# Kernel tuning notes

Measured on AMD Instinct MI355X. Metric: run time of the kernel, lower is better.

The kernel has to match this reference:

```python
import jax, jax.numpy as jnp
import numpy as np

EPS = 1e-8  # torch CosineSimilarity default eps


def setup_inputs() -> dict:
    key = jax.random.key(0)
    ks = jax.random.split(key, 7)
    B, C, W, E, D = 64, 256, 256, 2048, 2048
    return {
        "x_img_dense": jax.random.normal(ks[0], (B, C, E), dtype=jnp.float32),
        "x_txt_dense": jax.random.normal(ks[1], (B, W, E), dtype=jnp.float32),
        "y_what_card_leader_choose": jax.random.normal(ks[2], (B, C), dtype=jnp.float32),
        "W_img1": jax.random.normal(ks[3], (D, E), dtype=jnp.float32) * 0.02,
        "b_img1": jax.random.normal(ks[4], (D,), dtype=jnp.float32) * 0.02,
        "W_words1": jax.random.normal(ks[5], (D, E), dtype=jnp.float32) * 0.02,
        "b_words1": jax.random.normal(ks[6], (D,), dtype=jnp.float32) * 0.02,
    }


def reference(x_img_dense, x_txt_dense, y_what_card_leader_choose,
              W_img1, b_img1, W_words1, b_words1):
    # Default path: img_layer=True, words_layer=True, comb_layer=False,
    # same_img_words_layer=False, gumbel=False, inference=False.
    xi = jnp.einsum('bce,de->bcd', x_img_dense, W_img1) + b_img1   # [B, C, D]
    xt = jnp.einsum('bwe,de->bwd', x_txt_dense, W_words1) + b_words1  # [B, W, D]

    # gather leader card embedding per batch element
    idx = jnp.argmax(y_what_card_leader_choose, axis=1)            # [B]
    leader = jnp.take_along_axis(xi, idx[:, None, None], axis=1)[:, 0, :]  # [B, D]

    # cosine similarity (dim=2 in torch): leader broadcast over words axis
    dot = jnp.einsum('bd,bwd->bw', leader, xt)                     # [B, W]
    denom = jnp.linalg.norm(leader, axis=-1, keepdims=True) * jnp.linalg.norm(xt, axis=-1)
    logits = dot / jnp.maximum(denom, EPS)                         # [B, W]

    # module returns softmax of `logits` (logits_final is dead code)
    return jax.nn.softmax(logits, axis=1)
```

## Files before the change

kernel.cpp:

```cpp
#include <hip/hip_runtime.h>
#include <hip/hip_bf16.h>
#include <stdint.h>

typedef unsigned short u16;
typedef __bf16 bf16x8 __attribute__((ext_vector_type(8)));
typedef float  f32x4  __attribute__((ext_vector_type(4)));
typedef float  fvec4  __attribute__((ext_vector_type(4)));

constexpr int NB = 64;
constexpr int NC = 256;
constexpr int NW = 256;
constexpr int NE = 2048;
constexpr int ND = 2048;
constexpr int MROWS = NB * NW;

constexpr int BM = 128, BN = 128, BK = 64;
constexpr int KSPLIT = 4;
constexpr int KSLICE = NE / KSPLIT;

constexpr int BM2 = 256, BN2 = 256;
constexpr int NT_K = NE / BK;
constexpr int NSLOT2 = ND / BN2;
constexpr int NSLOT1 = ND / BN;

constexpr size_t OFF_IDX  = 0;
constexpr size_t OFF_PART = 256;
constexpr size_t OFF_DOTP = 2097408;
constexpr size_t OFF_SSQP = 3145984;
constexpr size_t OFF_WW   = 4194560;
constexpr size_t OFF_XT   = 12583168;
constexpr size_t NEED_FULL = OFF_XT + 67108864ull;

__device__ __forceinline__ u16 f2bf(float f) {
    uint32_t u = __float_as_uint(f);
    u += 0x7fffu + ((u >> 16) & 1u);
    return (u16)(u >> 16);
}

__global__ void k_conv_argmax(const float* __restrict__ a, u16* __restrict__ da, int n4a,
                              const float* __restrict__ b, u16* __restrict__ db, int n4b,
                              const float* __restrict__ y, int* __restrict__ idx) {
    if (blockIdx.x == 0) {
        int t = threadIdx.x;
        int row = t >> 2, c = t & 3;
        float best = -3.4e38f; int bi = 0;
        for (int k = 0; k < 64; ++k) {
            int j = c + k * 4;
            float v = y[row * NC + j];
            if (v > best) { best = v; bi = j; }
        }
        #pragma unroll
        for (int off = 1; off <= 2; off <<= 1) {
            float ov = __shfl_xor(best, off, 64);
            int   oi = __shfl_xor(bi,   off, 64);
            if (ov > best || (ov == best && oi < bi)) { best = ov; bi = oi; }
        }
        if (c == 0) idx[row] = bi;
        return;
    }
    int i0 = (blockIdx.x - 1) * blockDim.x + threadIdx.x;
    int stride = (gridDim.x - 1) * blockDim.x;
    int n4 = n4a + n4b;
    for (int i = i0; i < n4; i += stride) {
        const fvec4* sp; ushort4* dp; int j;
        if (i < n4a) { sp = (const fvec4*)a; dp = (ushort4*)da; j = i; }
        else         { sp = (const fvec4*)b; dp = (ushort4*)db; j = i - n4a; }
        fvec4 v = __builtin_nontemporal_load(&sp[j]);
        ushort4 o = { f2bf(v.x), f2bf(v.y), f2bf(v.z), f2bf(v.w) };
        dp[j] = o;
    }
}

__global__ __launch_bounds__(256) void k_gemm0(
    const float* __restrict__ ximg, const int* __restrict__ idx,
    const float* __restrict__ Wimg, float* __restrict__ part)
{
    __shared__ __align__(16) u16 sA[BM * BK];
    __shared__ __align__(16) u16 sB[BN * BK];
    __shared__ int s_idx[64];

    const int t  = threadIdx.x;
    const int l  = t & 63;
    const int wv = t >> 6;
    const int wm = wv >> 1, wn = wv & 1;

    const int nt = blockIdx.x >> 2, ks = blockIdx.x & 3;
    const int n0 = nt * BN;
    const int kbase = ks * KSLICE;

    if (t < 64) s_idx[t] = idx[t];

    f32x4 acc[4][4];
    #pragma unroll
    for (int i = 0; i < 4; ++i)
        #pragma unroll
        for (int j = 0; j < 4; ++j) acc[i][j] = (f32x4){0.f, 0.f, 0.f, 0.f};

    const int lr = l >> 3, lp = l & 7;

    for (int k0 = kbase; k0 < kbase + KSLICE; k0 += BK) {
        __syncthreads();
        #pragma unroll
        for (int i = 0; i < 4; ++i) {
            int r = wv * 32 + i * 8 + lr;
            int g = lp ^ (r & 7);
            if (r < 64) {
                const float* src = ximg + ((size_t)r * NC + s_idx[r]) * NE + k0 + g * 8;
                float4 v0 = *(const float4*)src;
                float4 v1 = *(const float4*)(src + 4);
                uint4 ov;
                ov.x = (uint32_t)f2bf(v0.x) | ((uint32_t)f2bf(v0.y) << 16);
                ov.y = (uint32_t)f2bf(v0.z) | ((uint32_t)f2bf(v0.w) << 16);
                ov.z = (uint32_t)f2bf(v1.x) | ((uint32_t)f2bf(v1.y) << 16);
                ov.w = (uint32_t)f2bf(v1.z) | ((uint32_t)f2bf(v1.w) << 16);
                *(uint4*)&sA[r * BK + lp * 8] = ov;
            } else {
                *(uint4*)&sA[r * BK + lp * 8] = (uint4){0, 0, 0, 0};
            }
        }
        #pragma unroll
        for (int i = 0; i < 4; ++i) {
            int r = wv * 32 + i * 8 + lr;
            int g = lp ^ (r & 7);
            const float* src = Wimg + (size_t)(n0 + r) * NE + k0 + g * 8;
            float4 v0 = *(const float4*)src;
            float4 v1 = *(const float4*)(src + 4);
            uint4 ov;
            ov.x = (uint32_t)f2bf(v0.x) | ((uint32_t)f2bf(v0.y) << 16);
            ov.y = (uint32_t)f2bf(v0.z) | ((uint32_t)f2bf(v0.w) << 16);
            ov.z = (uint32_t)f2bf(v1.x) | ((uint32_t)f2bf(v1.y) << 16);
            ov.w = (uint32_t)f2bf(v1.z) | ((uint32_t)f2bf(v1.w) << 16);
            *(uint4*)&sB[r * BK + lp * 8] = ov;
        }
        __syncthreads();

        #pragma unroll
        for (int kk = 0; kk < 2; ++kk) {
            bf16x8 af[4], bfr[4];
            #pragma unroll
            for (int mi = 0; mi < 4; ++mi) {
                int ra = wm * 64 + mi * 16 + (l & 15);
                int g  = kk * 4 + (l >> 4);
                int p  = g ^ (ra & 7);
                af[mi] = *(const bf16x8*)&sA[ra * BK + p * 8];
            }
            #pragma unroll
            for (int nj = 0; nj < 4; ++nj) {
                int rb = wn * 64 + nj * 16 + (l & 15);
                int g  = kk * 4 + (l >> 4);
                int p  = g ^ (rb & 7);
                bfr[nj] = *(const bf16x8*)&sB[rb * BK + p * 8];
            }
            #pragma unroll
            for (int mi = 0; mi < 4; ++mi)
                #pragma unroll
                for (int nj = 0; nj < 4; ++nj)
                    acc[mi][nj] = __builtin_amdgcn_mfma_f32_16x16x32_bf16(
                        af[mi], bfr[nj], acc[mi][nj], 0, 0, 0);
        }
    }

    if (wm == 0) {
        const int quad = l >> 4, lc = l & 15;
        #pragma unroll
        for (int mi = 0; mi < 4; ++mi)
            #pragma unroll
            for (int r = 0; r < 4; ++r) {
                int m = mi * 16 + quad * 4 + r;
                #pragma unroll
                for (int nj = 0; nj < 4; ++nj) {
                    int n = n0 + wn * 64 + nj * 16 + lc;
                    part[((size_t)ks * NB + m) * ND + n] = acc[mi][nj][r];
                }
            }
    }
}

#define GLD(sp, dp) __builtin_amdgcn_global_load_lds( \
    (const __attribute__((address_space(1))) void*)(sp), \
    (__attribute__((address_space(3))) void*)(dp), 16, 0, 0)

#define STAGE_HALF(srcbase, h, kt, dstarr) do { \
    const u16* _s = (srcbase) + (size_t)(h) * 128 * NE + (size_t)(kt) * BK; \
    u16* _d = &(dstarr)[(h) * 8192 + dst0]; \
    GLD(_s, _d); \
    GLD(_s + (size_t)64 * NE, _d + 4096); \
} while (0)

#define TILE(S, tt) do { \
    const u16* slA = &lds[S][0][0]; \
    const u16* slB = &lds[S][1][0]; \
    bf16x8 a[8][2], b[4][2]; \
     \
    _Pragma("unroll") for (int mi = 0; mi < 4; ++mi) a[mi][0] = *(const bf16x8*)&slA[arow + mi * 1024 + pk0]; \
    _Pragma("unroll") for (int nj = 0; nj < 4; ++nj) b[nj][0] = *(const bf16x8*)&slB[brow + nj * 1024 + pk0]; \
    _Pragma("unroll") for (int mi = 0; mi < 4; ++mi) a[mi][1] = *(const bf16x8*)&slA[arow + mi * 1024 + pk1]; \
    if ((tt) + 1 < NT_K) STAGE_HALF(Bsrc, 0, (tt) + 1, lds[(S) ^ 1][1]); \
    __builtin_amdgcn_s_setprio(1); \
    _Pragma("unroll") for (int mi = 0; mi < 4; ++mi) \
        _Pragma("unroll") for (int nj = 0; nj < 4; ++nj) \
            acc[mi][nj] = __builtin_amdgcn_mfma_f32_16x16x32_bf16(a[mi][0], b[nj][0], acc[mi][nj], 0, 0, 0); \
    __builtin_amdgcn_s_setprio(0); \
     \
    _Pragma("unroll") for (int mi = 4; mi < 8; ++mi) a[mi][0] = *(const bf16x8*)&slA[arow + mi * 1024 + pk0]; \
    _Pragma("unroll") for (int nj = 0; nj < 4; ++nj) b[nj][1] = *(const bf16x8*)&slB[brow + nj * 1024 + pk1]; \
    _Pragma("unroll") for (int mi = 4; mi < 8; ++mi) a[mi][1] = *(const bf16x8*)&slA[arow + mi * 1024 + pk1]; \
    if ((tt) + 1 < NT_K) STAGE_HALF(Bsrc, 1, (tt) + 1, lds[(S) ^ 1][1]); \
    __builtin_amdgcn_s_setprio(1); \
    _Pragma("unroll") for (int mi = 0; mi < 4; ++mi) \
        _Pragma("unroll") for (int nj = 0; nj < 4; ++nj) \
            acc[mi][nj] = __builtin_amdgcn_mfma_f32_16x16x32_bf16(a[mi][1], b[nj][1], acc[mi][nj], 0, 0, 0); \
    __builtin_amdgcn_s_setprio(0); \
    asm volatile("s_waitcnt lgkmcnt(0)" ::: "memory"); \
    __builtin_amdgcn_s_barrier(); \
     \
    if ((tt) + 2 < NT_K) STAGE_HALF(Asrc, 0, (tt) + 2, lds[S][0]); \
    __builtin_amdgcn_s_setprio(1); \
    _Pragma("unroll") for (int mi = 4; mi < 8; ++mi) \
        _Pragma("unroll") for (int nj = 0; nj < 4; ++nj) \
            acc[mi][nj] = __builtin_amdgcn_mfma_f32_16x16x32_bf16(a[mi][0], b[nj][0], acc[mi][nj], 0, 0, 0); \
    __builtin_amdgcn_s_setprio(0); \
     \
    if ((tt) + 2 < NT_K) STAGE_HALF(Asrc, 1, (tt) + 2, lds[S][0]); \
    __builtin_amdgcn_s_setprio(1); \
    _Pragma("unroll") for (int mi = 4; mi < 8; ++mi) \
        _Pragma("unroll") for (int nj = 0; nj < 4; ++nj) \
            acc[mi][nj] = __builtin_amdgcn_mfma_f32_16x16x32_bf16(a[mi][1], b[nj][1], acc[mi][nj], 0, 0, 0); \
    __builtin_amdgcn_s_setprio(0); \
    if ((tt) < NT_K - 2) { asm volatile("s_waitcnt vmcnt(4)" ::: "memory"); } \
    else                 { asm volatile("s_waitcnt vmcnt(0)" ::: "memory"); } \
    __builtin_amdgcn_s_barrier(); \
} while (0)

__global__ __launch_bounds__(512, 2) void k_gemm1_8ph(
    const u16* __restrict__ A, const u16* __restrict__ B,
    const float* __restrict__ bwrd, const float* __restrict__ bimg,
    const float* __restrict__ part,
    float* __restrict__ dotp, float* __restrict__ ssqp)
{
    __shared__ __align__(16) u16 lds[2][2][16384];

    const int t  = threadIdx.x;
    const int l  = t & 63;
    const int wv = t >> 6;
    const int wm = wv >> 2;
    const int wn = wv & 3;

    const int mt = blockIdx.x >> 3;
    const int nt = blockIdx.x & 7;
    const int m0 = mt * BM2, n0 = nt * BN2;

    const int r0 = t >> 3;
    const int ge = ((t & 7) ^ (r0 & 7)) * 8;
    const u16* Asrc = A + (size_t)(m0 + r0) * NE + ge;
    const u16* Bsrc = B + (size_t)(n0 + r0) * NE + ge;
    const int dst0 = wv * 512;

    const int lc16 = l & 15, khi = l >> 4, lx = l & 7;
    const int pk0 = (khi ^ lx) * 8;
    const int pk1 = ((4 + khi) ^ lx) * 8;
    const int arow = (wm * 128 + lc16) * 64;
    const int brow = (wn * 64 + lc16) * 64;

    f32x4 acc[8][4];
    #pragma unroll
    for (int i = 0; i < 8; ++i)
        #pragma unroll
        for (int j = 0; j < 4; ++j) acc[i][j] = (f32x4){0.f, 0.f, 0.f, 0.f};

    STAGE_HALF(Asrc, 0, 0, lds[0][0]);
    STAGE_HALF(Asrc, 1, 0, lds[0][0]);
    STAGE_HALF(Bsrc, 0, 0, lds[0][1]);
    STAGE_HALF(Bsrc, 1, 0, lds[0][1]);
    STAGE_HALF(Asrc, 0, 1, lds[1][0]);
    STAGE_HALF(Asrc, 1, 1, lds[1][0]);
    asm volatile("s_waitcnt vmcnt(4)" ::: "memory");
    __builtin_amdgcn_s_barrier();

    #pragma unroll 1
    for (int it = 0; it < NT_K / 2; ++it) {
        const int tt0 = it * 2;
        TILE(0, tt0);
        TILE(1, tt0 + 1);
    }

    const int quad = l >> 4, lc = l & 15;
    float bia[4], ldr[4];
    #pragma unroll
    for (int nj = 0; nj < 4; ++nj) {
        int n = n0 + wn * 64 + nj * 16 + lc;
        bia[nj] = bwrd[n];
        float ld = bimg[n];
        #pragma unroll
        for (int ks = 0; ks < KSPLIT; ++ks)
            ld += part[((size_t)ks * NB + mt) * ND + n];
        ldr[nj] = ld;
    }
    __syncthreads();
    float* sRed = (float*)&lds[0][0][0];
    #pragma unroll
    for (int mi = 0; mi < 8; ++mi) {
        #pragma unroll
        for (int r = 0; r < 4; ++r) {
            float pd = 0.f, ps = 0.f;
            #pragma unroll
            for (int nj = 0; nj < 4; ++nj) {
                float v = acc[mi][nj][r] + bia[nj];
                pd += ldr[nj] * v;
                ps += v * v;
            }
            #pragma unroll
            for (int off = 1; off <= 8; off <<= 1) {
                pd += __shfl_xor(pd, off, 64);
                ps += __shfl_xor(ps, off, 64);
            }
            if (lc == 0) {
                int row = mi * 16 + quad * 4 + r;
                sRed[(wm * 128 + row) * 4 + wn]        = pd;
                sRed[1024 + (wm * 128 + row) * 4 + wn] = ps;
            }
        }
    }
    __syncthreads();
    if (t < 256) {
        int m = m0 + t;
        const fvec4* s4 = (const fvec4*)sRed;
        fvec4 vd = s4[t], vs = s4[256 + t];
        dotp[(size_t)nt * MROWS + m] = vd.x + vd.y + vd.z + vd.w;
        ssqp[(size_t)nt * MROWS + m] = vs.x + vs.y + vs.z + vs.w;
    }
}

#undef TILE
#undef STAGE_HALF
#undef GLD

__global__ __launch_bounds__(256) void k_gemm1_f32(
    const float* __restrict__ Av, const float* __restrict__ Bv,
    const float* __restrict__ bwrd, const float* __restrict__ bimg,
    const float* __restrict__ part,
    float* __restrict__ dotp, float* __restrict__ ssqp)
{
    __shared__ __align__(16) u16 sA[BM * BK];
    __shared__ __align__(16) u16 sB[BN * BK];

    const int t  = threadIdx.x;
    const int l  = t & 63;
    const int wv = t >> 6;
    const int wm = wv >> 1, wn = wv & 1;

    const int mt = blockIdx.x >> 4;
    const int nt = blockIdx.x & 15;
    const int m0 = mt * BM, n0 = nt * BN;

    f32x4 acc[4][4];
    #pragma unroll
    for (int i = 0; i < 4; ++i)
        #pragma unroll
        for (int jj = 0; jj < 4; ++jj) acc[i][jj] = (f32x4){0.f, 0.f, 0.f, 0.f};

    const int lr = l >> 3, lp = l & 7;

    for (int k0 = 0; k0 < NE; k0 += BK) {
        __syncthreads();
        #pragma unroll
        for (int i = 0; i < 4; ++i) {
            int r = wv * 32 + i * 8 + lr;
            int g = lp ^ (r & 7);
            const float* src = Av + (size_t)(m0 + r) * NE + k0 + g * 8;
            float4 v0 = *(const float4*)src;
            float4 v1 = *(const float4*)(src + 4);
            uint4 ov;
            ov.x = (uint32_t)f2bf(v0.x) | ((uint32_t)f2bf(v0.y) << 16);
            ov.y = (uint32_t)f2bf(v0.z) | ((uint32_t)f2bf(v0.w) << 16);
            ov.z = (uint32_t)f2bf(v1.x) | ((uint32_t)f2bf(v1.y) << 16);
            ov.w = (uint32_t)f2bf(v1.z) | ((uint32_t)f2bf(v1.w) << 16);
            *(uint4*)&sA[r * BK + lp * 8] = ov;
        }
        #pragma unroll
        for (int i = 0; i < 4; ++i) {
            int r = wv * 32 + i * 8 + lr;
            int g = lp ^ (r & 7);
            const float* src = Bv + (size_t)(n0 + r) * NE + k0 + g * 8;
            float4 v0 = *(const float4*)src;
            float4 v1 = *(const float4*)(src + 4);
            uint4 ov;
            ov.x = (uint32_t)f2bf(v0.x) | ((uint32_t)f2bf(v0.y) << 16);
            ov.y = (uint32_t)f2bf(v0.z) | ((uint32_t)f2bf(v0.w) << 16);
            ov.z = (uint32_t)f2bf(v1.x) | ((uint32_t)f2bf(v1.y) << 16);
            ov.w = (uint32_t)f2bf(v1.z) | ((uint32_t)f2bf(v1.w) << 16);
            *(uint4*)&sB[r * BK + lp * 8] = ov;
        }
        __syncthreads();

        #pragma unroll
        for (int kk = 0; kk < 2; ++kk) {
            bf16x8 af[4], bfr[4];
            #pragma unroll
            for (int mi = 0; mi < 4; ++mi) {
                int ra = wm * 64 + mi * 16 + (l & 15);
                int g  = kk * 4 + (l >> 4);
                int p  = g ^ (ra & 7);
                af[mi] = *(const bf16x8*)&sA[ra * BK + p * 8];
            }
            #pragma unroll
            for (int nj = 0; nj < 4; ++nj) {
                int rb = wn * 64 + nj * 16 + (l & 15);
                int g  = kk * 4 + (l >> 4);
                int p  = g ^ (rb & 7);
                bfr[nj] = *(const bf16x8*)&sB[rb * BK + p * 8];
            }
            #pragma unroll
            for (int mi = 0; mi < 4; ++mi)
                #pragma unroll
                for (int nj = 0; nj < 4; ++nj)
                    acc[mi][nj] = __builtin_amdgcn_mfma_f32_16x16x32_bf16(
                        af[mi], bfr[nj], acc[mi][nj], 0, 0, 0);
        }
    }

    const int quad = l >> 4, lc = l & 15;
    const int bidx = m0 >> 8;
    float bia[4], ldr[4];
    #pragma unroll
    for (int nj = 0; nj < 4; ++nj) {
        int n = n0 + wn * 64 + nj * 16 + lc;
        bia[nj] = bwrd[n];
        float ld = bimg[n];
        #pragma unroll
        for (int ks = 0; ks < KSPLIT; ++ks)
            ld += part[((size_t)ks * NB + bidx) * ND + n];
        ldr[nj] = ld;
    }
    __syncthreads();
    float* sRed = (float*)sA;
    #pragma unroll
    for (int mi = 0; mi < 4; ++mi) {
        #pragma unroll
        for (int r = 0; r < 4; ++r) {
            float pd = 0.f, ps = 0.f;
            #pragma unroll
            for (int nj = 0; nj < 4; ++nj) {
                float v = acc[mi][nj][r] + bia[nj];
                pd += ldr[nj] * v;
                ps += v * v;
            }
            #pragma unroll
            for (int off = 1; off <= 8; off <<= 1) {
                pd += __shfl_xor(pd, off, 64);
                ps += __shfl_xor(ps, off, 64);
            }
            if (lc == 0) {
                int lm = mi * 16 + quad * 4 + r;
                sRed[(wm * 2 + wn) * 64 + lm]       = pd;
                sRed[256 + (wm * 2 + wn) * 64 + lm] = ps;
            }
        }
    }
    __syncthreads();
    if (t < 128) {
        int wmm = t >> 6, lm = t & 63;
        int m = m0 + wmm * 64 + lm;
        dotp[(size_t)nt * MROWS + m] =
            sRed[(wmm * 2 + 0) * 64 + lm] + sRed[(wmm * 2 + 1) * 64 + lm];
        ssqp[(size_t)nt * MROWS + m] =
            sRed[256 + (wmm * 2 + 0) * 64 + lm] + sRed[256 + (wmm * 2 + 1) * 64 + lm];
    }
}

__global__ void k_final(const float* __restrict__ part, const float* __restrict__ bimg,
                        const float* __restrict__ dotp, const float* __restrict__ ssqp,
                        float* __restrict__ out, int nslot) {
    int b = blockIdx.x, t = threadIdx.x;
    __shared__ float rsum[4], redm[4], reds[4];
    float s2 = 0.f;
    #pragma unroll
    for (int i = 0; i < 8; ++i) {
        int d = i * 256 + t;
        float ld = bimg[d];
        #pragma unroll
        for (int ks = 0; ks < KSPLIT; ++ks)
            ld += part[((size_t)ks * NB + b) * ND + d];
        s2 += ld * ld;
    }
    for (int off = 1; off < 64; off <<= 1) s2 += __shfl_xor(s2, off, 64);
    if ((t & 63) == 0) rsum[t >> 6] = s2;
    __syncthreads();
    float ln2 = rsum[0] + rsum[1] + rsum[2] + rsum[3];

    int m = b * NW + t;
    float dt = 0.f, sq = 0.f;
    for (int s = 0; s < nslot; ++s) {
        dt += dotp[(size_t)s * MROWS + m];
        sq += ssqp[(size_t)s * MROWS + m];
    }
    float dn = sqrtf(ln2) * sqrtf(sq);
    float lg = dt / fmaxf(dn, 1e-8f);
    float mx = lg;
    for (int off = 1; off < 64; off <<= 1) mx = fmaxf(mx, __shfl_xor(mx, off, 64));
    int wvi = t >> 6;
    if ((t & 63) == 0) redm[wvi] = mx;
    __syncthreads();
    mx = fmaxf(fmaxf(redm[0], redm[1]), fmaxf(redm[2], redm[3]));
    float e = __expf(lg - mx);
    float s = e;
    for (int off = 1; off < 64; off <<= 1) s += __shfl_xor(s, off, 64);
    if ((t & 63) == 0) reds[wvi] = s;
    __syncthreads();
    s = reds[0] + reds[1] + reds[2] + reds[3];
    out[m] = e / s;
}

extern "C" void kernel_launch(void* const* d_in, const int* in_sizes, int n_in,
                              void* d_out, int out_size, void* d_ws, size_t ws_size,
                              hipStream_t stream) {
    const float* ximg = (const float*)d_in[0];
    const float* xtxt = (const float*)d_in[1];
    const float* y    = (const float*)d_in[2];
    const float* Wimg = (const float*)d_in[3];
    const float* bimg = (const float*)d_in[4];
    const float* Wwrd = (const float*)d_in[5];
    const float* bwrd = (const float*)d_in[6];
    float* out = (float*)d_out;

    char* ws = (char*)d_ws;
    int*   idx  = (int*)(ws + OFF_IDX);
    float* part = (float*)(ws + OFF_PART);
    float* dotp = (float*)(ws + OFF_DOTP);
    float* ssqp = (float*)(ws + OFF_SSQP);
    u16*   WWb  = (u16*)(ws + OFF_WW);
    u16*   XTb  = (u16*)(ws + OFF_XT);

    const bool preconv = ws_size >= NEED_FULL;

    if (preconv) {
        k_conv_argmax<<<4097, 256, 0, stream>>>(Wwrd, WWb, ND * NE / 4,
                                                xtxt, XTb, MROWS * NE / 4, y, idx);
        k_gemm0<<<(ND / BN) * KSPLIT, 256, 0, stream>>>(ximg, idx, Wimg, part);
        k_gemm1_8ph<<<(MROWS / BM2) * (ND / BN2), 512, 0, stream>>>(
            XTb, WWb, bwrd, bimg, part, dotp, ssqp);
        k_final<<<NB, 256, 0, stream>>>(part, bimg, dotp, ssqp, out, NSLOT2);
    } else {
        k_conv_argmax<<<1, 256, 0, stream>>>(nullptr, nullptr, 0,
                                             nullptr, nullptr, 0, y, idx);
        k_gemm0<<<(ND / BN) * KSPLIT, 256, 0, stream>>>(ximg, idx, Wimg, part);
        k_gemm1_f32<<<(MROWS / BM) * (ND / BN), 256, 0, stream>>>(
            xtxt, Wwrd, bwrd, bimg, part, dotp, ssqp);
        k_final<<<NB, 256, 0, stream>>>(part, bimg, dotp, ssqp, out, NSLOT1);
    }
}
```

Baseline: 469.4 us.

## Simplify GEMM tile pipeline to single-stage prefetch with one barrier per tile

Restructures the main bf16 GEMM tile loop. The old version prefetched A two tiles ahead and used a fine-grained vmcnt/lgkmcnt schedule with two barriers per tile. The new version prefetches A and B only one tile ahead, uses smaller fragment register arrays, and ends each tile with a single __syncthreads. This cuts register pressure and scheduling complexity, but gives shallower load-latency hiding and a full-drain barrier each tile.

```diff
diff --git a/kernel.cpp b/kernel.cpp
--- a/kernel.cpp
+++ b/kernel.cpp
@@ -187,49 +187,45 @@
     GLD(_s + (size_t)64 * NE, _d + 4096); \
 } while (0)
 
+#define RD_A(dst, mibase, pk) \
+    _Pragma("unroll") for (int q = 0; q < 4; ++q) \
+        dst[q] = *(const bf16x8*)&slA[arow + ((mibase) + q) * 1024 + (pk)];
+
+#define RD_B(dst, pk) \
+    _Pragma("unroll") for (int q = 0; q < 4; ++q) \
+        dst[q] = *(const bf16x8*)&slB[brow + q * 1024 + (pk)];
+
+#define MM(accbase, afr, bfr) \
+    _Pragma("unroll") for (int q = 0; q < 4; ++q) \
+        _Pragma("unroll") for (int nj = 0; nj < 4; ++nj) \
+            acc[(accbase) + q][nj] = __builtin_amdgcn_mfma_f32_16x16x32_bf16( \
+                afr[q], bfr[nj], acc[(accbase) + q][nj], 0, 0, 0);
+
 #define TILE(S, tt) do { \
     const u16* slA = &lds[S][0][0]; \
     const u16* slB = &lds[S][1][0]; \
-    bf16x8 a[8][2], b[4][2]; \
+    bf16x8 af[4], bfr[4]; \
      \
-    _Pragma("unroll") for (int mi = 0; mi < 4; ++mi) a[mi][0] = *(const bf16x8*)&slA[arow + mi * 1024 + pk0]; \
-    _Pragma("unroll") for (int nj = 0; nj < 4; ++nj) b[nj][0] = *(const bf16x8*)&slB[brow + nj * 1024 + pk0]; \
-    _Pragma("unroll") for (int mi = 0; mi < 4; ++mi) a[mi][1] = *(const bf16x8*)&slA[arow + mi * 1024 + pk1]; \
-    if ((tt) + 1 < NT_K) STAGE_HALF(Bsrc, 0, (tt) + 1, lds[(S) ^ 1][1]); \
-    __builtin_amdgcn_s_setprio(1); \
-    _Pragma("unroll") for (int mi = 0; mi < 4; ++mi) \
-        _Pragma("unroll") for (int nj = 0; nj < 4; ++nj) \
-            acc[mi][nj] = __builtin_amdgcn_mfma_f32_16x16x32_bf16(a[mi][0], b[nj][0], acc[mi][nj], 0, 0, 0); \
-    __builtin_amdgcn_s_setprio(0); \
+    RD_A(af, 0, pk0); RD_B(bfr, pk0); \
+    if ((tt) + 1 < NT_K) { \
+        STAGE_HALF(Asrc, 0, (tt) + 1, lds[(S) ^ 1][0]); \
+        STAGE_HALF(Asrc, 1, (tt) + 1, lds[(S) ^ 1][0]); \
+    } \
+    __builtin_amdgcn_s_setprio(1); MM(0, af, bfr); __builtin_amdgcn_s_setprio(0); \
      \
-    _Pragma("unroll") for (int mi = 4; mi < 8; ++mi) a[mi][0] = *(const bf16x8*)&slA[arow + mi * 1024 + pk0]; \
-    _Pragma("unroll") for (int nj = 0; nj < 4; ++nj) b[nj][1] = *(const bf16x8*)&slB[brow + nj * 1024 + pk1]; \
-    _Pragma("unroll") for (int mi = 4; mi < 8; ++mi) a[mi][1] = *(const bf16x8*)&slA[arow + mi * 1024 + pk1]; \
-    if ((tt) + 1 < NT_K) STAGE_HALF(Bsrc, 1, (tt) + 1, lds[(S) ^ 1][1]); \
-    __builtin_amdgcn_s_setprio(1); \
-    _Pragma("unroll") for (int mi = 0; mi < 4; ++mi) \
-        _Pragma("unroll") for (int nj = 0; nj < 4; ++nj) \
-            acc[mi][nj] = __builtin_amdgcn_mfma_f32_16x16x32_bf16(a[mi][1], b[nj][1], acc[mi][nj], 0, 0, 0); \
-    __builtin_amdgcn_s_setprio(0); \
-    asm volatile("s_waitcnt lgkmcnt(0)" ::: "memory"); \
-    __builtin_amdgcn_s_barrier(); \
+    RD_A(af, 4, pk0); \
+    if ((tt) + 1 < NT_K) { \
+        STAGE_HALF(Bsrc, 0, (tt) + 1, lds[(S) ^ 1][1]); \
+        STAGE_HALF(Bsrc, 1, (tt) + 1, lds[(S) ^ 1][1]); \
+    } \
+    __builtin_amdgcn_s_setprio(1); MM(4, af, bfr); __builtin_amdgcn_s_setprio(0); \
      \
-    if ((tt) + 2 < NT_K) STAGE_HALF(Asrc, 0, (tt) + 2, lds[S][0]); \
-    __builtin_amdgcn_s_setprio(1); \
-    _Pragma("unroll") for (int mi = 4; mi < 8; ++mi) \
-        _Pragma("unroll") for (int nj = 0; nj < 4; ++nj) \
-            acc[mi][nj] = __builtin_amdgcn_mfma_f32_16x16x32_bf16(a[mi][0], b[nj][0], acc[mi][nj], 0, 0, 0); \
-    __builtin_amdgcn_s_setprio(0); \
+    RD_A(af, 0, pk1); RD_B(bfr, pk1); \
+    __builtin_amdgcn_s_setprio(1); MM(0, af, bfr); __builtin_amdgcn_s_setprio(0); \
      \
-    if ((tt) + 2 < NT_K) STAGE_HALF(Asrc, 1, (tt) + 2, lds[S][0]); \
-    __builtin_amdgcn_s_setprio(1); \
-    _Pragma("unroll") for (int mi = 4; mi < 8; ++mi) \
-        _Pragma("unroll") for (int nj = 0; nj < 4; ++nj) \
-            acc[mi][nj] = __builtin_amdgcn_mfma_f32_16x16x32_bf16(a[mi][1], b[nj][1], acc[mi][nj], 0, 0, 0); \
-    __builtin_amdgcn_s_setprio(0); \
-    if ((tt) < NT_K - 2) { asm volatile("s_waitcnt vmcnt(4)" ::: "memory"); } \
-    else                 { asm volatile("s_waitcnt vmcnt(0)" ::: "memory"); } \
-    __builtin_amdgcn_s_barrier(); \
+    RD_A(af, 4, pk1); \
+    __builtin_amdgcn_s_setprio(1); MM(4, af, bfr); __builtin_amdgcn_s_setprio(0); \
+    __syncthreads();    \
 } while (0)
 
 __global__ __launch_bounds__(512, 2) void k_gemm1_8ph(
@@ -272,16 +268,12 @@
     STAGE_HALF(Asrc, 1, 0, lds[0][0]);
     STAGE_HALF(Bsrc, 0, 0, lds[0][1]);
     STAGE_HALF(Bsrc, 1, 0, lds[0][1]);
-    STAGE_HALF(Asrc, 0, 1, lds[1][0]);
-    STAGE_HALF(Asrc, 1, 1, lds[1][0]);
-    asm volatile("s_waitcnt vmcnt(4)" ::: "memory");
-    __builtin_amdgcn_s_barrier();
+    __syncthreads();
 
     #pragma unroll 1
     for (int it = 0; it < NT_K / 2; ++it) {
-        const int tt0 = it * 2;
-        TILE(0, tt0);
-        TILE(1, tt0 + 1);
+        TILE(0, it * 2);
+        TILE(1, it * 2 + 1);
     }
 
     const int quad = l >> 4, lc = l & 15;
@@ -332,6 +324,9 @@
 }
 
 #undef TILE
+#undef MM
+#undef RD_B
+#undef RD_A
 #undef STAGE_HALF
 #undef GLD
 
```

Result: faster. 408.9 us (-12.9%).
